# Kernel tuning notes

Hardware: AMD Instinct MI355X
Metric: run time of the kernel (lower is better)

## Reference

```python
import jax, jax.numpy as jnp
import numpy as np

EPS = 1e-05
TEMP = 0.01
N_BINS = 15
N = 524288
C = 100


def setup_inputs() -> dict:
    key = jax.random.key(0)
    k1, k2 = jax.random.split(key)
    logits = jax.random.normal(k1, (N, C), dtype=jnp.float32)
    labels = jax.random.randint(k2, (N,), 0, C, dtype=jnp.int64)
    return {"logits": logits, "labels": labels}


def reference(logits, labels):
    # Faithful to torch: `predictions, confidences = torch.max(log_softmax, 1)`
    # -> predictions = max log-prob VALUES, confidences = argmax INDICES.
    logp = jax.nn.log_softmax(logits, axis=1)
    predictions = jnp.max(logp, axis=1)                      # [N] float
    confidences = jnp.argmax(logp, axis=1).astype(jnp.float32)  # [N] (indices as float)

    anchors = jnp.arange(1.0 / (2.0 * N_BINS), 1.0, 1.0 / N_BINS, dtype=jnp.float32)  # [B]

    # broadcasted -(c - a)^2 / temp, softmax over bins
    diff = -(confidences[:, None] - anchors[None, :]) ** 2 / TEMP  # [N, B]
    coeffs = jax.nn.softmax(diff, axis=1)                          # [N, B]

    sum_coeffs = jnp.sum(coeffs, axis=0)                           # [B]
    denom = jnp.maximum(sum_coeffs, EPS)

    bins_confidence = jnp.sum(confidences[:, None] * coeffs, axis=0) / denom

    accuracies = (predictions == labels.astype(predictions.dtype)).astype(jnp.float32)  # [N]
    bins_accuracy = jnp.sum(accuracies[:, None] * coeffs, axis=0) / denom

    # F.normalize(p=1): L1 normalization
    bin_weights = sum_coeffs / jnp.maximum(jnp.sum(jnp.abs(sum_coeffs)), EPS)

    ece = jnp.sqrt(jnp.dot((bins_confidence - bins_accuracy) ** 2, bin_weights))
    return ece
```

## Files before the change

kernel.cpp:

```cpp
#include <hip/hip_runtime.h>
#include <math.h>

#define NBINS 15
#define NCLS 100
#define ECE_EPS 1e-5f

__global__ __launch_bounds__(256) void ece_hist(const float* __restrict__ logits,
                                                const int* __restrict__ labels,
                                                int* __restrict__ g_cnt,
                                                float* __restrict__ g_acc,
                                                int n_rows) {
    __shared__ int   s_cnt[NCLS];
    __shared__ float s_accs[NCLS];
    const int tid = threadIdx.x;
    if (tid < NCLS) { s_cnt[tid] = 0; s_accs[tid] = 0.0f; }
    __syncthreads();

    const float4* __restrict__ lg4 = (const float4*)logits;
    const int stride = gridDim.x * blockDim.x;
    for (int row = blockIdx.x * blockDim.x + tid; row < n_rows; row += stride) {
        float4 v[25];
        const float4* __restrict__ p = lg4 + (long)row * 25;
        #pragma unroll
        for (int j = 0; j < 25; ++j) v[j] = p[j];

        float m = -INFINITY; int mi = 0;
        #pragma unroll
        for (int j = 0; j < 25; ++j) {
            if (v[j].x > m) { m = v[j].x; mi = 4 * j;     }
            if (v[j].y > m) { m = v[j].y; mi = 4 * j + 1; }
            if (v[j].z > m) { m = v[j].z; mi = 4 * j + 2; }
            if (v[j].w > m) { m = v[j].w; mi = 4 * j + 3; }
        }

        float s0 = 0.0f, s1 = 0.0f, s2 = 0.0f, s3 = 0.0f;
        #pragma unroll
        for (int j = 0; j < 25; ++j) {
            s0 += __expf(v[j].x - m);
            s1 += __expf(v[j].y - m);
            s2 += __expf(v[j].z - m);
            s3 += __expf(v[j].w - m);
        }
        const float s = (s0 + s1) + (s2 + s3);

        const float pred = -__logf(s);
        const float acc  = (pred == (float)labels[row]) ? 1.0f : 0.0f;

        atomicAdd(&s_cnt[mi], 1);
        if (acc != 0.0f) atomicAdd(&s_accs[mi], acc);
    }
    __syncthreads();
    if (tid < NCLS) {
        const int c = s_cnt[tid];
        if (c) atomicAdd(&g_cnt[tid], c);
        const float a = s_accs[tid];
        if (a != 0.0f) atomicAdd(&g_acc[tid], a);
    }
}

__global__ void ece_final(const int* __restrict__ g_cnt,
                          const float* __restrict__ g_acc,
                          float* __restrict__ out) {
    __shared__ float s_bins[3 * NBINS];
    const int tid = threadIdx.x;
    if (tid < 3 * NBINS) s_bins[tid] = 0.0f;
    __syncthreads();

    if (tid < NCLS) {
        const float cnt  = (float)g_cnt[tid];
        const float accv = g_acc[tid];
        const float conf = (float)tid;
        float diff[NBINS];
        float dm = -INFINITY;
        #pragma unroll
        for (int b = 0; b < NBINS; ++b) {
            const float a = (float)(2 * b + 1) * (1.0f / 30.0f);
            const float d = conf - a;
            diff[b] = -(d * d) * 100.0f;
            dm = fmaxf(dm, diff[b]);
        }
        float es = 0.0f;
        float e[NBINS];
        #pragma unroll
        for (int b = 0; b < NBINS; ++b) { e[b] = __expf(diff[b] - dm); es += e[b]; }
        const float inv = 1.0f / es;
        #pragma unroll
        for (int b = 0; b < NBINS; ++b) {
            const float coeff = e[b] * inv;
            if (coeff != 0.0f || cnt != 0.0f) {
                atomicAdd(&s_bins[b],             cnt * coeff);
                atomicAdd(&s_bins[NBINS + b],     conf * cnt * coeff);
                atomicAdd(&s_bins[2 * NBINS + b], accv * coeff);
            }
        }
    }
    __syncthreads();

    if (tid == 0) {
        float total = 0.0f;
        #pragma unroll
        for (int b = 0; b < NBINS; ++b) total += fabsf(s_bins[b]);
        const float invw = 1.0f / fmaxf(total, ECE_EPS);
        float ece = 0.0f;
        #pragma unroll
        for (int b = 0; b < NBINS; ++b) {
            const float sc = s_bins[b];
            const float denom = fmaxf(sc, ECE_EPS);
            const float bc = s_bins[NBINS + b] / denom;
            const float ba = s_bins[2 * NBINS + b] / denom;
            const float d  = bc - ba;
            ece += d * d * (sc * invw);
        }
        out[0] = sqrtf(ece);
    }
}

extern "C" void kernel_launch(void* const* d_in, const int* in_sizes, int n_in,
                              void* d_out, int out_size, void* d_ws, size_t ws_size,
                              hipStream_t stream) {
    const float* logits = (const float*)d_in[0];
    const int*   labels = (const int*)d_in[1];
    int*   g_cnt = (int*)d_ws;
    float* g_acc = (float*)((char*)d_ws + NCLS * sizeof(int));
    float* outp  = (float*)d_out;
    const int n_rows = in_sizes[1];

    hipMemsetAsync(d_ws, 0, NCLS * (sizeof(int) + sizeof(float)), stream);
    ece_hist<<<1024, 256, 0, stream>>>(logits, labels, g_cnt, g_acc, n_rows);
    ece_final<<<1, 128, 0, stream>>>(g_cnt, g_acc, outp);
}
```

Before: 379.8 us.

## Stage logit rows through LDS with direct global-to-LDS loads for coalescing

Replaces per-thread strided float4 row loads with wave-wide coalesced global_load_lds transfers into shared memory, then each lane reads its row from LDS. Blocks shrink to one 64-lane wave so no block barriers are needed, and the grid grows to 2048. A scalar tail path handles leftover rows. The per-row loads were uncoalesced (400-byte stride across lanes). The change trades that for an LDS round trip and a full waitcnt stall per chunk, with no double buffering.

```diff
diff --git a/kernel.cpp b/kernel.cpp
--- a/kernel.cpp
+++ b/kernel.cpp
@@ -5,24 +5,36 @@
 #define NCLS 100
 #define ECE_EPS 1e-5f
 
-__global__ __launch_bounds__(256) void ece_hist(const float* __restrict__ logits,
-                                                const int* __restrict__ labels,
-                                                int* __restrict__ g_cnt,
-                                                float* __restrict__ g_acc,
-                                                int n_rows) {
+__global__ __launch_bounds__(64) void ece_hist(const float* __restrict__ logits,
+                                               const int* __restrict__ labels,
+                                               int* __restrict__ g_cnt,
+                                               float* __restrict__ g_acc,
+                                               int n_rows) {
+    __shared__ float s_rows[64 * NCLS];
     __shared__ int   s_cnt[NCLS];
     __shared__ float s_accs[NCLS];
-    const int tid = threadIdx.x;
-    if (tid < NCLS) { s_cnt[tid] = 0; s_accs[tid] = 0.0f; }
-    __syncthreads();
 
-    const float4* __restrict__ lg4 = (const float4*)logits;
-    const int stride = gridDim.x * blockDim.x;
-    for (int row = blockIdx.x * blockDim.x + tid; row < n_rows; row += stride) {
+    const int lane = threadIdx.x;
+    #pragma unroll
+    for (int i = lane; i < NCLS; i += 64) { s_cnt[i] = 0; s_accs[i] = 0.0f; }
+
+    const int n_chunks = n_rows >> 6;
+    for (int chunk = blockIdx.x; chunk < n_chunks; chunk += gridDim.x) {
+        const float* gbase = logits + (size_t)chunk * (64 * NCLS);
+        #pragma unroll
+        for (int j = 0; j < 25; ++j) {
+            __builtin_amdgcn_global_load_lds(
+                (const __attribute__((address_space(1))) void*)(gbase + (size_t)(j * 64 + lane) * 4),
+                (__attribute__((address_space(3))) void*)(&s_rows[j * 256]),
+                16, 0, 0);
+        }
+        const int lab = labels[chunk * 64 + lane];
+        __builtin_amdgcn_s_waitcnt(0);
+
+        const float4* __restrict__ rp = (const float4*)&s_rows[lane * NCLS];
         float4 v[25];
-        const float4* __restrict__ p = lg4 + (long)row * 25;
         #pragma unroll
-        for (int j = 0; j < 25; ++j) v[j] = p[j];
+        for (int j = 0; j < 25; ++j) v[j] = rp[j];
 
         float m = -INFINITY; int mi = 0;
         #pragma unroll
@@ -32,7 +44,6 @@
             if (v[j].z > m) { m = v[j].z; mi = 4 * j + 2; }
             if (v[j].w > m) { m = v[j].w; mi = 4 * j + 3; }
         }
-
         float s0 = 0.0f, s1 = 0.0f, s2 = 0.0f, s3 = 0.0f;
         #pragma unroll
         for (int j = 0; j < 25; ++j) {
@@ -41,20 +52,28 @@
             s2 += __expf(v[j].z - m);
             s3 += __expf(v[j].w - m);
         }
-        const float s = (s0 + s1) + (s2 + s3);
-
-        const float pred = -__logf(s);
-        const float acc  = (pred == (float)labels[row]) ? 1.0f : 0.0f;
+        const float pred = -__logf((s0 + s1) + (s2 + s3));
 
         atomicAdd(&s_cnt[mi], 1);
-        if (acc != 0.0f) atomicAdd(&s_accs[mi], acc);
+        if (pred == (float)lab) atomicAdd(&s_accs[mi], 1.0f);
     }
-    __syncthreads();
-    if (tid < NCLS) {
-        const int c = s_cnt[tid];
-        if (c) atomicAdd(&g_cnt[tid], c);
-        const float a = s_accs[tid];
-        if (a != 0.0f) atomicAdd(&g_acc[tid], a);
+
+    const int tail_start = n_chunks << 6;
+    if (blockIdx.x == 0 && tail_start + lane < n_rows) {
+        const float* row = logits + (size_t)(tail_start + lane) * NCLS;
+        float m = -INFINITY; int mi = 0;
+        for (int c = 0; c < NCLS; ++c) { const float x = row[c]; if (x > m) { m = x; mi = c; } }
+        float s = 0.0f;
+        for (int c = 0; c < NCLS; ++c) s += __expf(row[c] - m);
+        const float pred = -__logf(s);
+        atomicAdd(&s_cnt[mi], 1);
+        if (pred == (float)labels[tail_start + lane]) atomicAdd(&s_accs[mi], 1.0f);
+    }
+
+    #pragma unroll
+    for (int i = lane; i < NCLS; i += 64) {
+        if (s_cnt[i])          atomicAdd(&g_cnt[i], s_cnt[i]);
+        if (s_accs[i] != 0.0f) atomicAdd(&g_acc[i], s_accs[i]);
     }
 }
 
@@ -87,11 +106,9 @@
         #pragma unroll
         for (int b = 0; b < NBINS; ++b) {
             const float coeff = e[b] * inv;
-            if (coeff != 0.0f || cnt != 0.0f) {
-                atomicAdd(&s_bins[b],             cnt * coeff);
-                atomicAdd(&s_bins[NBINS + b],     conf * cnt * coeff);
-                atomicAdd(&s_bins[2 * NBINS + b], accv * coeff);
-            }
+            atomicAdd(&s_bins[b],             cnt * coeff);
+            atomicAdd(&s_bins[NBINS + b],     conf * cnt * coeff);
+            atomicAdd(&s_bins[2 * NBINS + b], accv * coeff);
         }
     }
     __syncthreads();
@@ -126,6 +143,6 @@
     const int n_rows = in_sizes[1];
 
     hipMemsetAsync(d_ws, 0, NCLS * (sizeof(int) + sizeof(float)), stream);
-    ece_hist<<<1024, 256, 0, stream>>>(logits, labels, g_cnt, g_acc, n_rows);
+    ece_hist<<<2048, 64, 0, stream>>>(logits, labels, g_cnt, g_acc, n_rows);
     ece_final<<<1, 128, 0, stream>>>(g_cnt, g_acc, outp);
 }
```

New measurement: 380.2 us. No clear change (+0.1%).
